# Kernel tuning notes

Measured on AMD Instinct MI355X. Metric: run time of the kernel, lower is better.

Reference implementation:

```python
import jax, jax.numpy as jnp
import numpy as np


def log_g(x):
    # log(relu(x) + 0.5) for x >= 0, else -softplus(-x)
    pos = jnp.log(jnp.maximum(x, 0.0) + 0.5)
    neg = -jax.nn.softplus(-x)
    return jnp.where(x >= 0, pos, neg)


def parallel_scan_log(log_coeffs, log_values):
    # h_t = a_t * h_{t-1} + b_t, computed stably in log space
    a_star = jnp.cumsum(log_coeffs, axis=1)
    log_h0_plus_b_star = jax.lax.cumlogsumexp(log_values - a_star, axis=1)
    log_h = a_star + log_h0_plus_b_star
    return jnp.exp(log_h)


def setup_inputs() -> dict:
    key = jax.random.key(0)
    k1, k2 = jax.random.split(key)
    B, S, D = 8, 4096, 1024
    x = jax.random.normal(k1, (B, S, D), dtype=jnp.float32)
    # torch nn.Linear(dim, 2*inner_dim, bias=False): weight [2*inner_dim, dim]
    W_hg = jax.random.normal(k2, (2 * D, D), dtype=jnp.float32) * (1.0 / np.sqrt(D))
    return {"x": x, "W_hg": W_hg}


def reference(x, W_hg):
    # hidden_gate projection: [B,S,D] @ [D, 2*inner] -> [B,S,2*inner]
    hg = jnp.einsum("bsd,ed->bse", x, W_hg)
    hidden, gate = jnp.split(hg, 2, axis=-1)
    log_coeffs = -jax.nn.softplus(gate)       # log(1 - z)
    log_z = -jax.nn.softplus(-gate)           # log(z)
    log_tilde_h = log_g(hidden)
    log_values = log_z + log_tilde_h
    out = parallel_scan_log(log_coeffs, log_values)
    # expansion_factor == 1.0 -> self.out is Identity; dropout_prob == 0 -> Identity
    return out
```

## Files before the change

### kernel.cpp

```cpp
#include <hip/hip_runtime.h>

#define B_   8
#define S_   4096
#define D_   1024
#define M_   (B_ * S_)
#define N_   (2 * D_)
#define K_   D_
#define CCH  128
#define LCH  32

#define BK   64
#define NT   (K_ / BK)

typedef __attribute__((ext_vector_type(8))) short bf16x8;
typedef __attribute__((ext_vector_type(4))) float f32x4;

__device__ __forceinline__ unsigned short f2bf(float f) {
  union { float f; unsigned u; } v; v.f = f;
  unsigned u = v.u;
  u = u + 0x7fffu + ((u >> 16) & 1u);
  return (unsigned short)(u >> 16);
}
__device__ __forceinline__ float bf2f(unsigned short h) {
  union { unsigned u; float f; } v; v.u = ((unsigned)h) << 16;
  return v.f;
}
__device__ __forceinline__ float sigmoidf_(float x) {
  return 1.0f / (1.0f + __expf(-x));
}

#define GLL(src, dst) __builtin_amdgcn_global_load_lds(                     \
      (const __attribute__((address_space(1))) void*)(src),                 \
      (__attribute__((address_space(3))) void*)(dst), 16, 0, 0)

__global__ __launch_bounds__(256) void k_cvt(const float* __restrict__ in,
                                             unsigned short* __restrict__ out,
                                             int n4) {
  int i = blockIdx.x * 256 + threadIdx.x;
  const int stride = gridDim.x * 256;
  for (; i < n4; i += stride) {
    float4 v = reinterpret_cast<const float4*>(in)[i];
    ushort4 o;
    o.x = f2bf(v.x); o.y = f2bf(v.y); o.z = f2bf(v.z); o.w = f2bf(v.w);
    reinterpret_cast<ushort4*>(out)[i] = o;
  }
}

__global__ __launch_bounds__(512, 2) void k_gemm(const unsigned short* __restrict__ xb,
                                                 const unsigned short* __restrict__ wb,
                                                 unsigned short* __restrict__ Gp,
                                                 unsigned short* __restrict__ Zp) {
  __shared__ unsigned short lds[65536];
  const int tid = threadIdx.x;
  int wg = blockIdx.x;
  wg = (wg & 7) * 128 + (wg >> 3);
  const int bm = wg >> 3;
  const int bn = wg & 7;
  const int lane = tid & 63;
  const int wid = tid >> 6;
  const int wr = wid >> 2;
  const int wc = wid & 3;
  const int fr = lane & 15;
  const int hi = lane >> 4;
  const int f7 = fr & 7;

  const int srow = tid >> 3;
  const int sblk = tid & 7;
  const int scol = ((sblk ^ (srow & 7)) * 16);
  const char* aS = (const char*)xb + (size_t)(bm * 256 + srow) * 2048 + scol;
  const char* bS = (const char*)wb + (size_t)(bn * 256 + srow) * 2048 + scol;
  char* const ldsc = (char*)lds + (size_t)tid * 16;

#define STAGE_PAIR(srcbase, kbyte, bufbyte, region, C0)                      \
  GLL((srcbase) + (size_t)(C0) * 131072 + (kbyte),                           \
      ldsc + (bufbyte) + (region) + (C0) * 8192);                            \
  GLL((srcbase) + (size_t)((C0) + 1) * 131072 + (kbyte),                     \
      ldsc + (bufbyte) + (region) + ((C0) + 1) * 8192)

  f32x4 acc[8][4] = {};
  bf16x8 av[8], bv[4];

  STAGE_PAIR(aS, 0, 0, 0, 0);       STAGE_PAIR(aS, 0, 0, 0, 2);
  STAGE_PAIR(bS, 0, 0, 32768, 0);   STAGE_PAIR(bS, 0, 0, 32768, 2);
  STAGE_PAIR(aS, 128, 65536, 0, 0);     STAGE_PAIR(aS, 128, 65536, 0, 2);
  STAGE_PAIR(bS, 128, 65536, 32768, 0); STAGE_PAIR(bS, 128, 65536, 32768, 2);

  const int swz0 = (hi ^ f7) * 8;
  const int swz1 = ((4 + hi) ^ f7) * 8;

#define LOAD_FRAGS(Ab, Bb, SWZ)                                              \
  _Pragma("unroll") for (int m = 0; m < 8; ++m)                              \
    av[m] = *(const bf16x8*)&(Ab)[(wr * 128 + m * 16 + fr) * 64 + (SWZ)];    \
  _Pragma("unroll") for (int n = 0; n < 4; ++n)                              \
    bv[n] = *(const bf16x8*)&(Bb)[(wc * 64 + n * 16 + fr) * 64 + (SWZ)];

#define PHASE(M0)                                                            \
  __builtin_amdgcn_s_setprio(1);                                             \
  _Pragma("unroll") for (int m = (M0); m < (M0) + 2; ++m)                    \
    _Pragma("unroll") for (int n = 0; n < 4; ++n)                            \
      acc[m][n] = __builtin_amdgcn_mfma_f32_16x16x32_bf16(av[m], bv[n],      \
                                                          acc[m][n], 0, 0, 0); \
  __builtin_amdgcn_s_setprio(0);

#define PHASE4(M0)                                                           \
  __builtin_amdgcn_s_setprio(1);                                             \
  _Pragma("unroll") for (int m = (M0); m < (M0) + 4; ++m)                    \
    _Pragma("unroll") for (int n = 0; n < 4; ++n)                            \
      acc[m][n] = __builtin_amdgcn_mfma_f32_16x16x32_bf16(av[m], bv[n],      \
                                                          acc[m][n], 0, 0, 0); \
  __builtin_amdgcn_s_setprio(0);

  for (int t = 0; t < NT; ++t) {
    if (t < NT - 1) asm volatile("s_waitcnt vmcnt(8)\n\ts_barrier" ::: "memory");
    else            asm volatile("s_waitcnt vmcnt(0)\n\ts_barrier" ::: "memory");

    const unsigned short* Ab = &lds[(t & 1) << 15];
    const unsigned short* Bb = Ab + 16384;
    const int bufbyte = (t & 1) * 65536;
    const size_t kbyte = (size_t)(t + 2) * 128;

    LOAD_FRAGS(Ab, Bb, swz0);
    PHASE4(0);
    PHASE4(4);
    LOAD_FRAGS(Ab, Bb, swz1);
    asm volatile("s_waitcnt lgkmcnt(0)\n\ts_barrier" ::: "memory");

    if (t < NT - 2) { STAGE_PAIR(aS, kbyte, bufbyte, 0, 0); }
    PHASE(0);
    if (t < NT - 2) { STAGE_PAIR(aS, kbyte, bufbyte, 0, 2); }
    PHASE(2);
    if (t < NT - 2) { STAGE_PAIR(bS, kbyte, bufbyte, 32768, 0); }
    PHASE(4);
    if (t < NT - 2) { STAGE_PAIR(bS, kbyte, bufbyte, 32768, 2); }
    PHASE(6);
  }

  const int row0 = bm * 256 + wr * 128 + (hi << 2);
  const int col0 = bn * 256 + wc * 64 + fr;
  if (bn < 4) {
#pragma unroll
    for (int m = 0; m < 8; ++m)
#pragma unroll
      for (int n = 0; n < 4; ++n)
#pragma unroll
        for (int i = 0; i < 4; ++i) {
          float v = acc[m][n][i];
          float g = (v >= 0.0f) ? (v + 0.5f) : sigmoidf_(v);
          Gp[(size_t)(row0 + m * 16 + i) * 1024 + (col0 + n * 16)] = f2bf(g);
        }
  } else {
#pragma unroll
    for (int m = 0; m < 8; ++m)
#pragma unroll
      for (int n = 0; n < 4; ++n)
#pragma unroll
        for (int i = 0; i < 4; ++i) {
          float v = acc[m][n][i];
          Zp[(size_t)(row0 + m * 16 + i) * 1024 + (col0 + n * 16 - 1024)] = f2bf(sigmoidf_(v));
        }
  }
}

__global__ __launch_bounds__(256) void k_scan1(const unsigned short* __restrict__ Gp,
                                               const unsigned short* __restrict__ Zp,
                                               float* __restrict__ Ap,
                                               float* __restrict__ Hp) {
  const int gid = blockIdx.x * 256 + threadIdx.x;
  const int c = blockIdx.y;
  const int b = gid >> 8;
  const int d0 = (gid & 255) << 2;
  size_t base = ((size_t)b * S_ + (size_t)c * LCH) * 1024 + d0;
  float4 aP = {1.f, 1.f, 1.f, 1.f};
  float4 h  = {0.f, 0.f, 0.f, 0.f};
#pragma unroll 8
  for (int s = 0; s < LCH; ++s) {
    ushort4 zu = *reinterpret_cast<const ushort4*>(Zp + base);
    ushort4 gu = *reinterpret_cast<const ushort4*>(Gp + base);
    float z0 = bf2f(zu.x), z1 = bf2f(zu.y), z2 = bf2f(zu.z), z3 = bf2f(zu.w);
    float a0 = 1.f - z0,   a1 = 1.f - z1,   a2 = 1.f - z2,   a3 = 1.f - z3;
    h.x = fmaf(a0, h.x, z0 * bf2f(gu.x));
    h.y = fmaf(a1, h.y, z1 * bf2f(gu.y));
    h.z = fmaf(a2, h.z, z2 * bf2f(gu.z));
    h.w = fmaf(a3, h.w, z3 * bf2f(gu.w));
    aP.x *= a0; aP.y *= a1; aP.z *= a2; aP.w *= a3;
    base += 1024;
  }
  reinterpret_cast<float4*>(Ap)[(size_t)c * 2048 + gid] = aP;
  reinterpret_cast<float4*>(Hp)[(size_t)c * 2048 + gid] = h;
}

__global__ __launch_bounds__(256) void k_scan2(const float* __restrict__ Ap,
                                               const float* __restrict__ Hp,
                                               float* __restrict__ Cin) {
  const int gid = blockIdx.x * 256 + threadIdx.x;
  float4 carry = {0.f, 0.f, 0.f, 0.f};
  for (int c = 0; c < CCH; ++c) {
    reinterpret_cast<float4*>(Cin)[(size_t)c * 2048 + gid] = carry;
    float4 a = reinterpret_cast<const float4*>(Ap)[(size_t)c * 2048 + gid];
    float4 hh = reinterpret_cast<const float4*>(Hp)[(size_t)c * 2048 + gid];
    carry.x = fmaf(a.x, carry.x, hh.x);
    carry.y = fmaf(a.y, carry.y, hh.y);
    carry.z = fmaf(a.z, carry.z, hh.z);
    carry.w = fmaf(a.w, carry.w, hh.w);
  }
}

__global__ __launch_bounds__(256) void k_scan3(const unsigned short* __restrict__ Gp,
                                               const unsigned short* __restrict__ Zp,
                                               const float* __restrict__ Cin,
                                               float* __restrict__ out) {
  const int gid = blockIdx.x * 256 + threadIdx.x;
  const int c = blockIdx.y;
  const int b = gid >> 8;
  const int d0 = (gid & 255) << 2;
  size_t base = ((size_t)b * S_ + (size_t)c * LCH) * 1024 + d0;
  float4 h = reinterpret_cast<const float4*>(Cin)[(size_t)c * 2048 + gid];
#pragma unroll 8
  for (int s = 0; s < LCH; ++s) {
    ushort4 zu = *reinterpret_cast<const ushort4*>(Zp + base);
    ushort4 gu = *reinterpret_cast<const ushort4*>(Gp + base);
    float z0 = bf2f(zu.x), z1 = bf2f(zu.y), z2 = bf2f(zu.z), z3 = bf2f(zu.w);
    h.x = fmaf(1.f - z0, h.x, z0 * bf2f(gu.x));
    h.y = fmaf(1.f - z1, h.y, z1 * bf2f(gu.y));
    h.z = fmaf(1.f - z2, h.z, z2 * bf2f(gu.z));
    h.w = fmaf(1.f - z3, h.w, z3 * bf2f(gu.w));
    *reinterpret_cast<float4*>(out + base) = h;
    base += 1024;
  }
}

extern "C" void kernel_launch(void* const* d_in, const int* in_sizes, int n_in,
                              void* d_out, int out_size, void* d_ws, size_t ws_size,
                              hipStream_t stream) {
  const float* x = (const float*)d_in[0];
  const float* W = (const float*)d_in[1];
  float* out = (float*)d_out;

  unsigned char* w = (unsigned char*)d_ws;
  unsigned short* xb = (unsigned short*)(w);
  unsigned short* wb = (unsigned short*)(w + 67108864);
  unsigned short* Gp = (unsigned short*)(w + 67108864 + 4194304);
  unsigned short* Zp = (unsigned short*)(w + 67108864 + 4194304 + 67108864);
  float* Ap  = (float*)(w);
  float* Hp  = (float*)(w + 4194304);
  float* Cin = (float*)(w + 8388608);

  k_cvt<<<4096, 256, 0, stream>>>(x, xb, (M_ * K_) / 4);
  k_cvt<<<2048, 256, 0, stream>>>(W, wb, (N_ * K_) / 4);
  k_gemm<<<(M_ / 256) * (N_ / 256), 512, 0, stream>>>(xb, wb, Gp, Zp);
  k_scan1<<<dim3(8, CCH), 256, 0, stream>>>(Gp, Zp, Ap, Hp);
  k_scan2<<<8, 256, 0, stream>>>(Ap, Hp, Cin);
  k_scan3<<<dim3(8, CCH), 256, 0, stream>>>(Gp, Zp, Cin, out);
}
```

Before: 265.2 us.

## Restructure GEMM main loop into 4-phase 1-ahead prefetch with smaller A fragments

Replaces the two-tile-ahead staging with single-tile-ahead double buffering, issuing global-to-LDS loads for the next K tile interleaved across four MFMA phases of sixteen ops each. A fragments are now loaded in halves of 4 registers instead of 8, which reduces register pressure. The loop also adds more barriers per iteration and waits for all outstanding global loads at the end of each tile. The aim is a finer-grained overlap of LDS reads, global prefetch and MFMA work, at the cost of a shallower prefetch depth and more synchronisation.

```diff
diff --git a/kernel.cpp b/kernel.cpp
--- a/kernel.cpp
+++ b/kernel.cpp
@@ -65,74 +65,77 @@
   const int f7 = fr & 7;
 
   const int srow = tid >> 3;
-  const int sblk = tid & 7;
-  const int scol = ((sblk ^ (srow & 7)) * 16);
+  const int scol = ((tid & 7) ^ (srow & 7)) * 16;
   const char* aS = (const char*)xb + (size_t)(bm * 256 + srow) * 2048 + scol;
   const char* bS = (const char*)wb + (size_t)(bn * 256 + srow) * 2048 + scol;
   char* const ldsc = (char*)lds + (size_t)tid * 16;
 
-#define STAGE_PAIR(srcbase, kbyte, bufbyte, region, C0)                      \
-  GLL((srcbase) + (size_t)(C0) * 131072 + (kbyte),                           \
-      ldsc + (bufbyte) + (region) + (C0) * 8192);                            \
-  GLL((srcbase) + (size_t)((C0) + 1) * 131072 + (kbyte),                     \
-      ldsc + (bufbyte) + (region) + ((C0) + 1) * 8192)
-
-  f32x4 acc[8][4] = {};
-  bf16x8 av[8], bv[4];
-
-  STAGE_PAIR(aS, 0, 0, 0, 0);       STAGE_PAIR(aS, 0, 0, 0, 2);
-  STAGE_PAIR(bS, 0, 0, 32768, 0);   STAGE_PAIR(bS, 0, 0, 32768, 2);
-  STAGE_PAIR(aS, 128, 65536, 0, 0);     STAGE_PAIR(aS, 128, 65536, 0, 2);
-  STAGE_PAIR(bS, 128, 65536, 32768, 0); STAGE_PAIR(bS, 128, 65536, 32768, 2);
-
   const int swz0 = (hi ^ f7) * 8;
   const int swz1 = ((4 + hi) ^ f7) * 8;
 
-#define LOAD_FRAGS(Ab, Bb, SWZ)                                              \
-  _Pragma("unroll") for (int m = 0; m < 8; ++m)                              \
-    av[m] = *(const bf16x8*)&(Ab)[(wr * 128 + m * 16 + fr) * 64 + (SWZ)];    \
+  f32x4 acc[8][4] = {};
+  bf16x8 av[4], bv[4];
+
+#define RD_BV(SWZ)                                                           \
   _Pragma("unroll") for (int n = 0; n < 4; ++n)                              \
-    bv[n] = *(const bf16x8*)&(Bb)[(wc * 64 + n * 16 + fr) * 64 + (SWZ)];
-
-#define PHASE(M0)                                                            \
+    bv[n] = *(const bf16x8*)&Bb[(wc * 64 + n * 16 + fr) * 64 + (SWZ)];
+#define RD_AV(MB, SWZ)                                                       \
+  _Pragma("unroll") for (int m = 0; m < 4; ++m)                              \
+    av[m] = *(const bf16x8*)&Ab[(wr * 128 + (MB) * 64 + m * 16 + fr) * 64 + (SWZ)];
+
+#define STAGE4(srcbase, region)                                              \
+  if (st) {                                                                  \
+    GLL((srcbase) + kb,                  ldsc + bufN + (region));            \
+    GLL((srcbase) + 131072 + kb,         ldsc + bufN + (region) + 8192);     \
+    GLL((srcbase) + 262144 + kb,         ldsc + bufN + (region) + 16384);    \
+    GLL((srcbase) + 393216 + kb,         ldsc + bufN + (region) + 24576);    \
+  }
+
+#define PHASE16(M0)                                                          \
+  __builtin_amdgcn_s_barrier();                                              \
+  asm volatile("s_waitcnt lgkmcnt(0)" ::: "memory");                         \
   __builtin_amdgcn_s_setprio(1);                                             \
-  _Pragma("unroll") for (int m = (M0); m < (M0) + 2; ++m)                    \
+  _Pragma("unroll") for (int m = 0; m < 4; ++m)                              \
     _Pragma("unroll") for (int n = 0; n < 4; ++n)                            \
-      acc[m][n] = __builtin_amdgcn_mfma_f32_16x16x32_bf16(av[m], bv[n],      \
-                                                          acc[m][n], 0, 0, 0); \
+      acc[(M0) + m][n] = __builtin_amdgcn_mfma_f32_16x16x32_bf16(            \
+          av[m], bv[n], acc[(M0) + m][n], 0, 0, 0);                          \
   __builtin_amdgcn_s_setprio(0);
 
-#define PHASE4(M0)                                                           \
-  __builtin_amdgcn_s_setprio(1);                                             \
-  _Pragma("unroll") for (int m = (M0); m < (M0) + 4; ++m)                    \
-    _Pragma("unroll") for (int n = 0; n < 4; ++n)                            \
-      acc[m][n] = __builtin_amdgcn_mfma_f32_16x16x32_bf16(av[m], bv[n],      \
-                                                          acc[m][n], 0, 0, 0); \
-  __builtin_amdgcn_s_setprio(0);
+#pragma unroll
+  for (int c = 0; c < 4; ++c) {
+    GLL(aS + (size_t)c * 131072, ldsc + c * 8192);
+    GLL(bS + (size_t)c * 131072, ldsc + 32768 + c * 8192);
+  }
+  asm volatile("s_waitcnt vmcnt(0)" ::: "memory");
+  __builtin_amdgcn_s_barrier();
 
   for (int t = 0; t < NT; ++t) {
-    if (t < NT - 1) asm volatile("s_waitcnt vmcnt(8)\n\ts_barrier" ::: "memory");
-    else            asm volatile("s_waitcnt vmcnt(0)\n\ts_barrier" ::: "memory");
-
     const unsigned short* Ab = &lds[(t & 1) << 15];
     const unsigned short* Bb = Ab + 16384;
-    const int bufbyte = (t & 1) * 65536;
-    const size_t kbyte = (size_t)(t + 2) * 128;
-
-    LOAD_FRAGS(Ab, Bb, swz0);
-    PHASE4(0);
-    PHASE4(4);
-    LOAD_FRAGS(Ab, Bb, swz1);
-    asm volatile("s_waitcnt lgkmcnt(0)\n\ts_barrier" ::: "memory");
-
-    if (t < NT - 2) { STAGE_PAIR(aS, kbyte, bufbyte, 0, 0); }
-    PHASE(0);
-    if (t < NT - 2) { STAGE_PAIR(aS, kbyte, bufbyte, 0, 2); }
-    PHASE(2);
-    if (t < NT - 2) { STAGE_PAIR(bS, kbyte, bufbyte, 32768, 0); }
-    PHASE(4);
-    if (t < NT - 2) { STAGE_PAIR(bS, kbyte, bufbyte, 32768, 2); }
-    PHASE(6);
+    const int bufN = ((t + 1) & 1) << 16;
+    const size_t kb = (size_t)(t + 1) * 128;
+    const bool st = (t < NT - 1);
+
+    RD_BV(swz0);
+    RD_AV(0, swz0);
+    STAGE4(aS, 0);
+    PHASE16(0);
+    __builtin_amdgcn_s_barrier();
+
+    RD_AV(1, swz0);
+    STAGE4(bS, 32768);
+    PHASE16(4);
+    __builtin_amdgcn_s_barrier();
+
+    RD_BV(swz1);
+    RD_AV(0, swz1);
+    PHASE16(0);
+    __builtin_amdgcn_s_barrier();
+
+    RD_AV(1, swz1);
+    PHASE16(4);
+    asm volatile("s_waitcnt vmcnt(0)" ::: "memory");
+    __builtin_amdgcn_s_barrier();
   }
 
   const int row0 = bm * 256 + wr * 128 + (hi << 2);
```

After: 273.9 us. 1.03x slower.
